# Kernel optimization log

Hardware: AMD Instinct MI355X
Metric: run time of the kernel (lower is better)

The kernel has to match this reference:

```python
import jax, jax.numpy as jnp
import numpy as np

B, S, D, H, FF = 2, 4096, 1024, 16, 4096
HD = D // H


def _layernorm(x, g, b, eps=1e-5):
    mu = jnp.mean(x, axis=-1, keepdims=True)
    var = jnp.var(x, axis=-1, keepdims=True)
    return (x - mu) * jax.lax.rsqrt(var + eps) * g + b


def setup_inputs() -> dict:
    key = jax.random.key(0)
    ks = jax.random.split(key, 20)
    sd = 1.0 / np.sqrt(D)
    sf = 1.0 / np.sqrt(FF)
    inp = {
        "x": jax.random.normal(ks[0], (B, S, D), jnp.float32),
        # attention projections, stored as [in, out]
        "wq": jax.random.normal(ks[1], (D, D), jnp.float32) * sd,
        "bq": jnp.zeros((D,), jnp.float32),
        "wk": jax.random.normal(ks[2], (D, D), jnp.float32) * sd,
        "bk": jnp.zeros((D,), jnp.float32),
        "wv": jax.random.normal(ks[3], (D, D), jnp.float32) * sd,
        "bv": jnp.zeros((D,), jnp.float32),
        "wo": jax.random.normal(ks[4], (D, D), jnp.float32) * sd,
        "bo": jnp.zeros((D,), jnp.float32),
        # block norm1 (pre-attention)
        "ln1_g": jnp.ones((D,), jnp.float32),
        "ln1_b": jnp.zeros((D,), jnp.float32),
        # FFN internal norm
        "lnf_g": jnp.ones((D,), jnp.float32),
        "lnf_b": jnp.zeros((D,), jnp.float32),
        # gated FFN
        "w1": jax.random.normal(ks[5], (D, FF), jnp.float32) * sd,
        "b1": jnp.zeros((FF,), jnp.float32),
        "wg": jax.random.normal(ks[6], (D, FF), jnp.float32) * sd,
        "bg": jnp.zeros((FF,), jnp.float32),
        "w2": jax.random.normal(ks[7], (FF, D), jnp.float32) * sf,
        "b2": jnp.zeros((D,), jnp.float32),
    }
    return inp


def reference(x, wq, bq, wk, bk, wv, bv, wo, bo, ln1_g, ln1_b,
              lnf_g, lnf_b, w1, b1, wg, bg, w2, b2):
    # pre-norm attention
    residual = x
    h = _layernorm(x, ln1_g, ln1_b)
    q = (h @ wq + bq).reshape(B, S, H, HD).transpose(0, 2, 1, 3)  # [B,H,S,hd]
    k = (h @ wk + bk).reshape(B, S, H, HD).transpose(0, 2, 1, 3)
    v = (h @ wv + bv).reshape(B, S, H, HD).transpose(0, 2, 1, 3)
    scores = jnp.einsum("bhqd,bhkd->bhqk", q, k) / np.sqrt(HD)
    attn = jax.nn.softmax(scores, axis=-1)  # [B,H,S,S] materialized as in torch src
    ctx = jnp.einsum("bhqk,bhkd->bhqd", attn, v)
    ctx = ctx.transpose(0, 2, 1, 3).reshape(B, S, D)
    attn_out = ctx @ wo + bo
    x = residual + attn_out  # dropout = 0 (eval)

    # gated FFN with internal pre-norm and residual
    res2 = x
    h2 = _layernorm(x, lnf_g, lnf_b)
    gate = jax.nn.sigmoid(h2 @ wg + bg)
    up = jax.nn.gelu(h2 @ w1 + b1, approximate=False)
    out = (up * gate) @ w2 + b2
    return out + res2
```

## Files before the change

kernel.cpp:

```cpp
#include <hip/hip_runtime.h>
#include <hip/hip_bf16.h>

#define BB 2
#define SS 4096
#define DD 1024
#define HH 16
#define HD 64
#define FF 4096
#define MM (BB*SS)

typedef __hip_bfloat16 bf16;
typedef __attribute__((ext_vector_type(8))) __bf16 v8bf;
typedef __attribute__((ext_vector_type(4))) float f32x4;
typedef __attribute__((ext_vector_type(16))) float f32x16;
typedef __attribute__((ext_vector_type(8))) unsigned short u16v8;

__device__ __forceinline__ f32x4 mfma16(v8bf a, v8bf b, f32x4 c) {
  return __builtin_amdgcn_mfma_f32_16x16x32_bf16(a, b, c, 0, 0, 0);
}
__device__ __forceinline__ f32x16 mfma32(v8bf a, v8bf b, f32x16 c) {
  return __builtin_amdgcn_mfma_f32_32x32x16_bf16(a, b, c, 0, 0, 0);
}
__device__ __forceinline__ void gload16(const void* g, void* l) {
  __builtin_amdgcn_global_load_lds((const __attribute__((address_space(1))) void*)g,
                                   (__attribute__((address_space(3))) void*)l, 16, 0, 0);
}
__device__ __forceinline__ unsigned cvtpk_bf16(float lo, float hi) {
  unsigned r;
  asm("v_cvt_pk_bf16_f32 %0, %1, %2" : "=v"(r) : "v"(lo), "v"(hi));
  return r;
}

__global__ void k_tcvt(const float* __restrict__ W, bf16* __restrict__ Wt, int K, int N)
{
  __shared__ float tile[32][33];
  const int n0 = blockIdx.x * 32, k0 = blockIdx.y * 32;
  const int tx = threadIdx.x, ty = threadIdx.y;
#pragma unroll
  for (int i = 0; i < 32; i += 8)
    tile[ty + i][tx] = W[(long)(k0 + ty + i) * N + n0 + tx];
  __syncthreads();
#pragma unroll
  for (int i = 0; i < 32; i += 8)
    Wt[(long)(n0 + ty + i) * K + k0 + tx] = __float2bfloat16(tile[tx][ty + i]);
}

__global__ __launch_bounds__(256)
void k_layernorm(const float* __restrict__ x, const float* __restrict__ g,
                 const float* __restrict__ b, bf16* __restrict__ out)
{
  const int row = blockIdx.x;
  const float4 v = ((const float4*)(x + (long)row * DD))[threadIdx.x];
  float s  = v.x + v.y + v.z + v.w;
  float s2 = v.x*v.x + v.y*v.y + v.z*v.z + v.w*v.w;
#pragma unroll
  for (int off = 1; off < 64; off <<= 1) {
    s  += __shfl_xor(s,  off);
    s2 += __shfl_xor(s2, off);
  }
  __shared__ float red[8];
  if ((threadIdx.x & 63) == 0) {
    red[threadIdx.x >> 6]       = s;
    red[(threadIdx.x >> 6) + 4] = s2;
  }
  __syncthreads();
  s  = red[0] + red[1] + red[2] + red[3];
  s2 = red[4] + red[5] + red[6] + red[7];
  const float mu = s * (1.f / DD);
  const float rs = rsqrtf(s2 * (1.f / DD) - mu * mu + 1e-5f);
  const float4 gv = ((const float4*)g)[threadIdx.x];
  const float4 bv = ((const float4*)b)[threadIdx.x];
  bf16* op = out + (long)row * DD + threadIdx.x * 4;
  op[0] = __float2bfloat16((v.x - mu) * rs * gv.x + bv.x);
  op[1] = __float2bfloat16((v.y - mu) * rs * gv.y + bv.y);
  op[2] = __float2bfloat16((v.z - mu) * rs * gv.z + bv.z);
  op[3] = __float2bfloat16((v.w - mu) * rs * gv.w + bv.w);
}

template<int EPI>
__global__ __launch_bounds__(256, 2)
void k_gemm(const bf16* __restrict__ A, const bf16* __restrict__ Bt,
            const float* __restrict__ bias, const float* __restrict__ res,
            void* __restrict__ Cout, int M, int N, int K, float scale)
{
  __shared__ __align__(16) bf16 As[128 * 32];
  __shared__ __align__(16) bf16 Bs[128 * 32];
  const int t = threadIdx.x;
  const int lane = t & 63, w = t >> 6;
  const int wr = w >> 1, wc = w & 1;
  const int fr = lane & 15, fq = lane >> 4;
  const long m0 = (long)blockIdx.y * 128, n0 = (long)blockIdx.x * 128;

  f32x4 acc[4][4] = {};

  const bf16* Ag0 = A  + (m0 + (t >> 2)) * K + (t & 3) * 8;
  const bf16* Ag1 = Ag0 + 64L * K;
  const bf16* Bg0 = Bt + (n0 + (t >> 2)) * K + (t & 3) * 8;
  const bf16* Bg1 = Bg0 + 64L * K;
  bf16* Al0 = As + t * 8;
  bf16* Al1 = As + 2048 + t * 8;
  bf16* Bl0 = Bs + t * 8;
  bf16* Bl1 = Bs + 2048 + t * 8;

  for (int kk = 0; kk < K; kk += 32) {
    gload16(Ag0 + kk, Al0);
    gload16(Ag1 + kk, Al1);
    gload16(Bg0 + kk, Bl0);
    gload16(Bg1 + kk, Bl1);
    __syncthreads();
    v8bf af[4], bfr[4];
#pragma unroll
    for (int mt = 0; mt < 4; ++mt)
      af[mt] = *(const v8bf*)&As[(wr*64 + mt*16 + fr) * 32 + fq*8];
#pragma unroll
    for (int nt = 0; nt < 4; ++nt)
      bfr[nt] = *(const v8bf*)&Bs[(wc*64 + nt*16 + fr) * 32 + fq*8];
#pragma unroll
    for (int mt = 0; mt < 4; ++mt)
#pragma unroll
      for (int nt = 0; nt < 4; ++nt)
        acc[mt][nt] = mfma16(af[mt], bfr[nt], acc[mt][nt]);
    __syncthreads();
  }

#pragma unroll
  for (int nt = 0; nt < 4; ++nt) {
    const long col = n0 + wc*64 + nt*16 + fr;
    const float bv = bias[col];
#pragma unroll
    for (int mt = 0; mt < 4; ++mt) {
#pragma unroll
      for (int j = 0; j < 4; ++j) {
        const long row = m0 + wr*64 + mt*16 + fq*4 + j;
        float v = (acc[mt][nt][j] + bv) * scale;
        if (EPI == 0) {
          ((bf16*)Cout)[row * N + col] = __float2bfloat16(v);
        } else if (EPI == 1) {
          ((float*)Cout)[row * N + col] = v + res[row * N + col];
        } else {
          const long s = row & (SS - 1), bb = row >> 12;
          ((bf16*)Cout)[((bb * HH + (col >> 6)) * HD + (col & 63)) * (long)SS + s] =
              __float2bfloat16(v);
        }
      }
    }
  }
}

__global__ __launch_bounds__(256, 2)
void k_ffn_dual(const bf16* __restrict__ A, const bf16* __restrict__ BgT,
                const bf16* __restrict__ BuT, const float* __restrict__ bgb,
                const float* __restrict__ bub, bf16* __restrict__ Out)
{
  __shared__ __align__(16) bf16 As[128 * 32];
  __shared__ __align__(16) bf16 Gs[64 * 32];
  __shared__ __align__(16) bf16 Us[64 * 32];
  const int t = threadIdx.x;
  const int lane = t & 63, w = t >> 6;
  const int wr = w >> 1, wc = w & 1;
  const int fr = lane & 15, fq = lane >> 4;
  const long m0 = (long)blockIdx.y * 128, n0 = (long)blockIdx.x * 64;
  const int K = DD;

  f32x4 ag[4][2] = {}, au[4][2] = {};

  const bf16* Ag0 = A   + (m0 + (t >> 2)) * K + (t & 3) * 8;
  const bf16* Ag1 = Ag0 + 64L * K;
  const bf16* Gg  = BgT + (n0 + (t >> 2)) * K + (t & 3) * 8;
  const bf16* Ug  = BuT + (n0 + (t >> 2)) * K + (t & 3) * 8;

  for (int kk = 0; kk < K; kk += 32) {
    gload16(Ag0 + kk, As + t * 8);
    gload16(Ag1 + kk, As + 2048 + t * 8);
    gload16(Gg + kk, Gs + t * 8);
    gload16(Ug + kk, Us + t * 8);
    __syncthreads();
    v8bf af[4], gf[2], uf[2];
#pragma unroll
    for (int mt = 0; mt < 4; ++mt)
      af[mt] = *(const v8bf*)&As[(wr*64 + mt*16 + fr) * 32 + fq*8];
#pragma unroll
    for (int nt = 0; nt < 2; ++nt) {
      gf[nt] = *(const v8bf*)&Gs[(wc*32 + nt*16 + fr) * 32 + fq*8];
      uf[nt] = *(const v8bf*)&Us[(wc*32 + nt*16 + fr) * 32 + fq*8];
    }
#pragma unroll
    for (int mt = 0; mt < 4; ++mt)
#pragma unroll
      for (int nt = 0; nt < 2; ++nt) {
        ag[mt][nt] = mfma16(af[mt], gf[nt], ag[mt][nt]);
        au[mt][nt] = mfma16(af[mt], uf[nt], au[mt][nt]);
      }
    __syncthreads();
  }

#pragma unroll
  for (int nt = 0; nt < 2; ++nt) {
    const long col = n0 + wc*32 + nt*16 + fr;
    const float gb = bgb[col], ub = bub[col];
#pragma unroll
    for (int mt = 0; mt < 4; ++mt) {
#pragma unroll
      for (int j = 0; j < 4; ++j) {
        const long row = m0 + wr*64 + mt*16 + fq*4 + j;
        const float g = ag[mt][nt][j] + gb;
        const float u = au[mt][nt][j] + ub;
        const float sg = 1.f / (1.f + __expf(-g));
        const float gl = 0.5f * u * (1.f + erff(u * 0.70710678118f));
        Out[row * FF + col] = __float2bfloat16(sg * gl);
      }
    }
  }
}

__global__ __launch_bounds__(256, 2)
void k_attn(const bf16* __restrict__ Qb, const bf16* __restrict__ Kb,
            const bf16* __restrict__ Vt, bf16* __restrict__ ctx)
{
  __shared__ __align__(16) bf16 Ksh[2][4096];
  __shared__ __align__(16) bf16 Vsh[2][4096];
  const int t = threadIdx.x;
  const int lane = t & 63, w = t >> 6;
  const int q5 = lane & 31, hi = lane >> 5;
  const int q0 = blockIdx.x * 128;
  const int h = blockIdx.y, b = blockIdx.z;
  const long qk_base = ((long)b * SS) * DD + h * HD;
  const long vt_base = ((long)(b * HH + h)) * ((long)HD * SS);

  const int r0 = t >> 3;
  const int cswz = ((t & 7) * 16) ^ ((r0 & 7) << 4);
  const bf16* kg = Kb + qk_base + (long)r0 * DD + (cswz >> 1);
  const bf16* vg = Vt + vt_base + (long)r0 * SS + (cswz >> 1);

  v8bf qf[4];
  {
    const bf16* qp = Qb + qk_base + (long)(q0 + w * 32 + q5) * DD + hi * 8;
#pragma unroll
    for (int c = 0; c < 4; ++c) qf[c] = *(const v8bf*)(qp + c * 16);
  }

  int kcol[4];
#pragma unroll
  for (int c = 0; c < 4; ++c)
    kcol[c] = ((c * 32 + hi * 16) ^ ((q5 & 7) << 4)) >> 1;

  float m_ = -1e30f, l_ = 0.f;
  f32x16 o0 = {}, o1 = {};

#define STAGE(bufidx, kv0_) do {                                  \
    const bf16* kp_ = kg + (long)(kv0_) * DD;                     \
    gload16(kp_,            &Ksh[bufidx][t * 8]);                 \
    gload16(kp_ + 32L * DD, &Ksh[bufidx][2048 + t * 8]);          \
    const bf16* vp_ = vg + (kv0_);                                \
    gload16(vp_,            &Vsh[bufidx][t * 8]);                 \
    gload16(vp_ + 32L * SS, &Vsh[bufidx][2048 + t * 8]);          \
  } while (0)

  STAGE(0, 0);
  __syncthreads();

  for (int tt = 0; tt < SS / 64; ++tt) {
    const int cur = tt & 1;
    if (tt + 1 < SS / 64) STAGE(cur ^ 1, (tt + 1) * 64);

    f32x16 s0 = {}, s1 = {};
#pragma unroll
    for (int c = 0; c < 4; ++c) {
      const v8bf k0 = *(const v8bf*)&Ksh[cur][q5 * 64 + kcol[c]];
      const v8bf k1 = *(const v8bf*)&Ksh[cur][(32 + q5) * 64 + kcol[c]];
      s0 = mfma32(k0, qf[c], s0);
      s1 = mfma32(k1, qf[c], s1);
    }

    float pm = s0[0];
#pragma unroll
    for (int r = 1; r < 16; ++r) pm = fmaxf(pm, s0[r]);
#pragma unroll
    for (int r = 0; r < 16; ++r) pm = fmaxf(pm, s1[r]);
    pm = fmaxf(pm, __shfl_xor(pm, 32));
    const float mn = fmaxf(m_, pm);
    const float al = __builtin_amdgcn_exp2f(m_ - mn);
    m_ = mn;
    float rs = 0.f;
#pragma unroll
    for (int r = 0; r < 16; ++r) { s0[r] = __builtin_amdgcn_exp2f(s0[r] - mn); rs += s0[r]; }
#pragma unroll
    for (int r = 0; r < 16; ++r) { s1[r] = __builtin_amdgcn_exp2f(s1[r] - mn); rs += s1[r]; }
    rs += __shfl_xor(rs, 32);
    l_ = l_ * al + rs;
#pragma unroll
    for (int r = 0; r < 16; ++r) { o0[r] *= al; o1[r] *= al; }

    v8bf pb[4];
#pragma unroll
    for (int c = 0; c < 4; ++c) {
      const int base = (c & 1) * 8;
      unsigned wa0, wa1, wb0, wb1;
      if (c < 2) {
        wa0 = cvtpk_bf16(s0[base + 0], s0[base + 1]);
        wa1 = cvtpk_bf16(s0[base + 2], s0[base + 3]);
        wb0 = cvtpk_bf16(s0[base + 4], s0[base + 5]);
        wb1 = cvtpk_bf16(s0[base + 6], s0[base + 7]);
      } else {
        wa0 = cvtpk_bf16(s1[base + 0], s1[base + 1]);
        wa1 = cvtpk_bf16(s1[base + 2], s1[base + 3]);
        wb0 = cvtpk_bf16(s1[base + 4], s1[base + 5]);
        wb1 = cvtpk_bf16(s1[base + 6], s1[base + 7]);
      }
      asm("v_permlane32_swap_b32 %0, %1" : "+v"(wa0), "+v"(wb0));
      asm("v_permlane32_swap_b32 %0, %1" : "+v"(wa1), "+v"(wb1));
      union { unsigned u[4]; v8bf v; } cvt;
      cvt.u[0] = wa0; cvt.u[1] = wa1; cvt.u[2] = wb0; cvt.u[3] = wb1;
      pb[c] = cvt.v;
    }

#pragma unroll
    for (int c = 0; c < 4; ++c) {
      const v8bf v0f = *(const v8bf*)&Vsh[cur][q5 * 64 + kcol[c]];
      const v8bf v1f = *(const v8bf*)&Vsh[cur][(32 + q5) * 64 + kcol[c]];
      o0 = mfma32(v0f, pb[c], o0);
      o1 = mfma32(v1f, pb[c], o1);
    }
    __syncthreads();
  }
#undef STAGE

  const float inv = 1.f / l_;
  bf16* Osh = &Ksh[0][0];
  const int qrow = w * 32 + q5;
  const int oswz = (qrow & 7) << 4;
#pragma unroll
  for (int r = 0; r < 16; ++r) {
    const int d0 = (r & 3) + 8 * (r >> 2) + 4 * hi;
    Osh[((qrow * 128 + d0 * 2) ^ oswz) >> 1]        = __float2bfloat16(o0[r] * inv);
    Osh[((qrow * 128 + (32 + d0) * 2) ^ oswz) >> 1] = __float2bfloat16(o1[r] * inv);
  }
  __syncthreads();
  {
    const int q = t >> 1, half = t & 1;
    const int qs = (q & 7) << 4;
    bf16* cp = ctx + qk_base + (long)(q0 + q) * DD + half * 32;
#pragma unroll
    for (int s = 0; s < 4; ++s) {
      const int byte = (q * 128 + half * 64 + s * 16) ^ qs;
      *(u16v8*)(cp + s * 8) = *(const u16v8*)&Osh[byte >> 1];
    }
  }
}

extern "C" void kernel_launch(void* const* d_in, const int* in_sizes, int n_in,
                              void* d_out, int out_size, void* d_ws, size_t ws_size,
                              hipStream_t stream)
{
  const float* x    = (const float*)d_in[0];
  const float* wq   = (const float*)d_in[1];
  const float* bq   = (const float*)d_in[2];
  const float* wk   = (const float*)d_in[3];
  const float* bk   = (const float*)d_in[4];
  const float* wv   = (const float*)d_in[5];
  const float* bv   = (const float*)d_in[6];
  const float* wo   = (const float*)d_in[7];
  const float* bo   = (const float*)d_in[8];
  const float* ln1g = (const float*)d_in[9];
  const float* ln1b = (const float*)d_in[10];
  const float* lnfg = (const float*)d_in[11];
  const float* lnfb = (const float*)d_in[12];
  const float* w1   = (const float*)d_in[13];
  const float* b1   = (const float*)d_in[14];
  const float* wg   = (const float*)d_in[15];
  const float* bg   = (const float*)d_in[16];
  const float* w2   = (const float*)d_in[17];
  const float* b2   = (const float*)d_in[18];

  char* ws = (char*)d_ws;
  const size_t MB = 1u << 20;
  bf16*  WqT  = (bf16*)(ws + 0 * MB);
  bf16*  WkT  = (bf16*)(ws + 2 * MB);
  bf16*  WvT  = (bf16*)(ws + 4 * MB);
  bf16*  WoT  = (bf16*)(ws + 6 * MB);
  bf16*  W1T  = (bf16*)(ws + 8 * MB);
  bf16*  WgT  = (bf16*)(ws + 16 * MB);
  bf16*  W2T  = (bf16*)(ws + 24 * MB);
  float* x1   = (float*)(ws + 32 * MB);
  bf16*  hbuf = (bf16*)(ws + 64 * MB);
  bf16*  Qb   = (bf16*)(ws + 80 * MB);
  bf16*  Kb   = (bf16*)(ws + 96 * MB);
  bf16*  Vtb  = (bf16*)(ws + 112 * MB);
  bf16*  ctxb = (bf16*)(ws + 128 * MB);
  bf16*  prod = (bf16*)(ws + 80 * MB);

  dim3 tb(32, 8);
  k_tcvt<<<dim3(32, 32), tb, 0, stream>>>(wq, WqT, 1024, 1024);
  k_tcvt<<<dim3(32, 32), tb, 0, stream>>>(wk, WkT, 1024, 1024);
  k_tcvt<<<dim3(32, 32), tb, 0, stream>>>(wv, WvT, 1024, 1024);
  k_tcvt<<<dim3(32, 32), tb, 0, stream>>>(wo, WoT, 1024, 1024);
  k_tcvt<<<dim3(128, 32), tb, 0, stream>>>(w1, W1T, 1024, 4096);
  k_tcvt<<<dim3(128, 32), tb, 0, stream>>>(wg, WgT, 1024, 4096);
  k_tcvt<<<dim3(32, 128), tb, 0, stream>>>(w2, W2T, 4096, 1024);

  k_layernorm<<<MM, 256, 0, stream>>>(x, ln1g, ln1b, hbuf);

  const float qscale = 0.1803368801111204f;
  dim3 g1(1024 / 128, MM / 128);
  k_gemm<0><<<g1, 256, 0, stream>>>(hbuf, WqT, bq, nullptr, Qb, MM, 1024, 1024, qscale);
  k_gemm<0><<<g1, 256, 0, stream>>>(hbuf, WkT, bk, nullptr, Kb, MM, 1024, 1024, 1.f);
  k_gemm<2><<<g1, 256, 0, stream>>>(hbuf, WvT, bv, nullptr, Vtb, MM, 1024, 1024, 1.f);

  k_attn<<<dim3(SS / 128, HH, BB), 256, 0, stream>>>(Qb, Kb, Vtb, ctxb);

  k_gemm<1><<<g1, 256, 0, stream>>>(ctxb, WoT, bo, x, x1, MM, 1024, 1024, 1.f);

  k_layernorm<<<MM, 256, 0, stream>>>(x1, lnfg, lnfb, hbuf);

  k_ffn_dual<<<dim3(FF / 64, MM / 128), 256, 0, stream>>>(hbuf, WgT, W1T, bg, b1, prod);

  k_gemm<1><<<g1, 256, 0, stream>>>(prod, W2T, b2, x1, (float*)d_out, MM, 1024, 4096, 1.f);
}
```

Before: 637.6 us.

## Widen FFN dual GEMM tile and transpose V in a separate kernel

The FFN dual gate/up GEMM tile grows from 128x64 to 128x128 per block, doubling accumulators per wave so each A tile load feeds twice as many MFMAs and A is re-read from global memory half as often. The V projection now writes a plain row-major output, and a new LDS-tiled kernel transposes it into the per-head [d][s] layout with vectorized stores. This replaces the old scattered 2-byte strided epilogue writes. The cost is one extra kernel launch plus an extra read and write of V, and higher register pressure in the FFN kernel, which could hurt occupancy under launch_bounds(256,2). ctx also now reuses hbuf.

```diff
diff --git a/kernel.cpp b/kernel.cpp
--- a/kernel.cpp
+++ b/kernel.cpp
@@ -43,6 +43,35 @@
 #pragma unroll
   for (int i = 0; i < 32; i += 8)
     Wt[(long)(n0 + ty + i) * K + k0 + tx] = __float2bfloat16(tile[tx][ty + i]);
+}
+
+__global__ __launch_bounds__(256)
+void k_vtrans(const bf16* __restrict__ V, bf16* __restrict__ Vt)
+{
+  __shared__ bf16 tile[64][72];
+  const int s0 = blockIdx.x * 64;
+  const int h  = blockIdx.y;
+  const int b  = blockIdx.z;
+  const int t  = threadIdx.x;
+  const int r = t >> 3, c8 = t & 7;
+#pragma unroll
+  for (int it = 0; it < 2; ++it) {
+    const int sr = it * 32 + r;
+    const u16v8 v = *(const u16v8*)(V + (long)(b * SS + s0 + sr) * DD + h * 64 + c8 * 8);
+#pragma unroll
+    for (int e = 0; e < 8; ++e)
+      ((unsigned short*)&tile[sr][0])[c8 * 8 + e] = v[e];
+  }
+  __syncthreads();
+#pragma unroll
+  for (int it = 0; it < 2; ++it) {
+    const int d = it * 32 + r;
+    union { unsigned short s[8]; u16v8 v; } o;
+#pragma unroll
+    for (int e = 0; e < 8; ++e)
+      o.s[e] = ((const unsigned short*)tile)[(c8 * 8 + e) * 72 + d];
+    *(u16v8*)(Vt + ((long)(b * HH + h) * HD + d) * (long)SS + s0 + c8 * 8) = o.v;
+  }
 }
 
 __global__ __launch_bounds__(256)
@@ -135,12 +164,8 @@
         float v = (acc[mt][nt][j] + bv) * scale;
         if (EPI == 0) {
           ((bf16*)Cout)[row * N + col] = __float2bfloat16(v);
-        } else if (EPI == 1) {
+        } else {
           ((float*)Cout)[row * N + col] = v + res[row * N + col];
-        } else {
-          const long s = row & (SS - 1), bb = row >> 12;
-          ((bf16*)Cout)[((bb * HH + (col >> 6)) * HD + (col & 63)) * (long)SS + s] =
-              __float2bfloat16(v);
         }
       }
     }
@@ -153,41 +178,45 @@
                 const float* __restrict__ bub, bf16* __restrict__ Out)
 {
   __shared__ __align__(16) bf16 As[128 * 32];
-  __shared__ __align__(16) bf16 Gs[64 * 32];
-  __shared__ __align__(16) bf16 Us[64 * 32];
+  __shared__ __align__(16) bf16 Gs[128 * 32];
+  __shared__ __align__(16) bf16 Us[128 * 32];
   const int t = threadIdx.x;
   const int lane = t & 63, w = t >> 6;
   const int wr = w >> 1, wc = w & 1;
   const int fr = lane & 15, fq = lane >> 4;
-  const long m0 = (long)blockIdx.y * 128, n0 = (long)blockIdx.x * 64;
+  const long m0 = (long)blockIdx.y * 128, n0 = (long)blockIdx.x * 128;
   const int K = DD;
 
-  f32x4 ag[4][2] = {}, au[4][2] = {};
+  f32x4 ag[4][4] = {}, au[4][4] = {};
 
   const bf16* Ag0 = A   + (m0 + (t >> 2)) * K + (t & 3) * 8;
   const bf16* Ag1 = Ag0 + 64L * K;
-  const bf16* Gg  = BgT + (n0 + (t >> 2)) * K + (t & 3) * 8;
-  const bf16* Ug  = BuT + (n0 + (t >> 2)) * K + (t & 3) * 8;
+  const bf16* Gg0 = BgT + (n0 + (t >> 2)) * K + (t & 3) * 8;
+  const bf16* Gg1 = Gg0 + 64L * K;
+  const bf16* Ug0 = BuT + (n0 + (t >> 2)) * K + (t & 3) * 8;
+  const bf16* Ug1 = Ug0 + 64L * K;
 
   for (int kk = 0; kk < K; kk += 32) {
     gload16(Ag0 + kk, As + t * 8);
     gload16(Ag1 + kk, As + 2048 + t * 8);
-    gload16(Gg + kk, Gs + t * 8);
-    gload16(Ug + kk, Us + t * 8);
+    gload16(Gg0 + kk, Gs + t * 8);
+    gload16(Gg1 + kk, Gs + 2048 + t * 8);
+    gload16(Ug0 + kk, Us + t * 8);
+    gload16(Ug1 + kk, Us + 2048 + t * 8);
     __syncthreads();
-    v8bf af[4], gf[2], uf[2];
+    v8bf af[4], gf[4], uf[4];
 #pragma unroll
     for (int mt = 0; mt < 4; ++mt)
       af[mt] = *(const v8bf*)&As[(wr*64 + mt*16 + fr) * 32 + fq*8];
 #pragma unroll
-    for (int nt = 0; nt < 2; ++nt) {
-      gf[nt] = *(const v8bf*)&Gs[(wc*32 + nt*16 + fr) * 32 + fq*8];
-      uf[nt] = *(const v8bf*)&Us[(wc*32 + nt*16 + fr) * 32 + fq*8];
+    for (int nt = 0; nt < 4; ++nt) {
+      gf[nt] = *(const v8bf*)&Gs[(wc*64 + nt*16 + fr) * 32 + fq*8];
+      uf[nt] = *(const v8bf*)&Us[(wc*64 + nt*16 + fr) * 32 + fq*8];
     }
 #pragma unroll
     for (int mt = 0; mt < 4; ++mt)
 #pragma unroll
-      for (int nt = 0; nt < 2; ++nt) {
+      for (int nt = 0; nt < 4; ++nt) {
         ag[mt][nt] = mfma16(af[mt], gf[nt], ag[mt][nt]);
         au[mt][nt] = mfma16(af[mt], uf[nt], au[mt][nt]);
       }
@@ -195,8 +224,8 @@
   }
 
 #pragma unroll
-  for (int nt = 0; nt < 2; ++nt) {
-    const long col = n0 + wc*32 + nt*16 + fr;
+  for (int nt = 0; nt < 4; ++nt) {
+    const long col = n0 + wc*64 + nt*16 + fr;
     const float gb = bgb[col], ub = bub[col];
 #pragma unroll
     for (int mt = 0; mt < 4; ++mt) {
@@ -385,8 +414,9 @@
   bf16*  hbuf = (bf16*)(ws + 64 * MB);
   bf16*  Qb   = (bf16*)(ws + 80 * MB);
   bf16*  Kb   = (bf16*)(ws + 96 * MB);
-  bf16*  Vtb  = (bf16*)(ws + 112 * MB);
-  bf16*  ctxb = (bf16*)(ws + 128 * MB);
+  bf16*  Vb   = (bf16*)(ws + 112 * MB);
+  bf16*  Vtb  = (bf16*)(ws + 128 * MB);
+  bf16*  ctxb = hbuf;
   bf16*  prod = (bf16*)(ws + 80 * MB);
 
   dim3 tb(32, 8);
@@ -404,7 +434,8 @@
   dim3 g1(1024 / 128, MM / 128);
   k_gemm<0><<<g1, 256, 0, stream>>>(hbuf, WqT, bq, nullptr, Qb, MM, 1024, 1024, qscale);
   k_gemm<0><<<g1, 256, 0, stream>>>(hbuf, WkT, bk, nullptr, Kb, MM, 1024, 1024, 1.f);
-  k_gemm<2><<<g1, 256, 0, stream>>>(hbuf, WvT, bv, nullptr, Vtb, MM, 1024, 1024, 1.f);
+  k_gemm<0><<<g1, 256, 0, stream>>>(hbuf, WvT, bv, nullptr, Vb, MM, 1024, 1024, 1.f);
+  k_vtrans<<<dim3(SS / 64, HH, BB), 256, 0, stream>>>(Vb, Vtb);
 
   k_attn<<<dim3(SS / 128, HH, BB), 256, 0, stream>>>(Qb, Kb, Vtb, ctxb);
 
@@ -412,7 +443,7 @@
 
   k_layernorm<<<MM, 256, 0, stream>>>(x1, lnfg, lnfb, hbuf);
 
-  k_ffn_dual<<<dim3(FF / 64, MM / 128), 256, 0, stream>>>(hbuf, WgT, W1T, bg, b1, prod);
+  k_ffn_dual<<<dim3(FF / 128, MM / 128), 256, 0, stream>>>(hbuf, WgT, W1T, bg, b1, prod);
 
   k_gemm<1><<<g1, 256, 0, stream>>>(prod, W2T, b2, x1, (float*)d_out, MM, 1024, 4096, 1.f);
 }
```

After: 659.8 us. +3.5%, slower.
